# Performance work log

Measured on AMD Instinct MI355X. Metric: run time of the kernel, lower is better.

The kernel has to match this reference:

```python
import jax, jax.numpy as jnp
import numpy as np

B, S, V, F, H = 256, 512, 50000, 64, 256


def setup_inputs() -> dict:
    key = jax.random.key(0)
    ks = jax.random.split(key, 12)
    s_in = 1.0 / np.sqrt(F)
    s_hid = 1.0 / np.sqrt(H)
    return {
        "batch": jax.random.randint(ks[0], (B, S), 0, V),
        "features": jax.random.normal(ks[1], (V, F), jnp.float32),
        "W_ih0": jax.random.normal(ks[2], (H, F), jnp.float32) * s_in,
        "W_hh0": jax.random.normal(ks[3], (H, H), jnp.float32) * s_hid,
        "b_ih0": jax.random.normal(ks[4], (H,), jnp.float32) * s_hid,
        "b_hh0": jax.random.normal(ks[5], (H,), jnp.float32) * s_hid,
        "W_ih1": jax.random.normal(ks[6], (H, H), jnp.float32) * s_hid,
        "W_hh1": jax.random.normal(ks[7], (H, H), jnp.float32) * s_hid,
        "b_ih1": jax.random.normal(ks[8], (H,), jnp.float32) * s_hid,
        "b_hh1": jax.random.normal(ks[9], (H,), jnp.float32) * s_hid,
        "W_out": jax.random.normal(ks[10], (V, H), jnp.float32) * s_hid,
        "b_out": jax.random.normal(ks[11], (V,), jnp.float32) * s_hid,
    }


def _rnn_layer(x, W_ih, W_hh, b_ih, b_hh):
    # x: [B, S, Din] -> [B, S, H]; torch tanh RNN: h_t = tanh(x_t W_ih^T + b_ih + h_{t-1} W_hh^T + b_hh)
    xW = jnp.einsum('bsd,hd->bsh', x, W_ih) + (b_ih + b_hh)  # precompute input projection
    h0 = jnp.zeros((x.shape[0], W_hh.shape[0]), x.dtype)

    def step(h, xt):
        h = jnp.tanh(xt + h @ W_hh.T)
        return h, h

    _, ys = jax.lax.scan(step, h0, jnp.swapaxes(xW, 0, 1))  # scan over time
    return jnp.swapaxes(ys, 0, 1)


def reference(batch, features, W_ih0, W_hh0, b_ih0, b_hh0,
              W_ih1, W_hh1, b_ih1, b_hh1, W_out, b_out):
    # vectorized replacement of the nested per-token gather loop
    full_representation = features[batch]            # [B, S, F]
    h = _rnn_layer(full_representation, W_ih0, W_hh0, b_ih0, b_hh0)
    h = _rnn_layer(h, W_ih1, W_hh1, b_ih1, b_hh1)    # [B, S, H]
    return h[:, -1, :] @ W_out.T + b_out             # [B, V]
```

## Files before the change

kernel.cpp:

```cpp
#include <hip/hip_runtime.h>

#define B_ 256
#define S_ 512
#define V_ 50000
#define F_ 64
#define H_ 256

typedef _Float16 f16;
typedef _Float16 f16x2 __attribute__((ext_vector_type(2)));
typedef _Float16 f16x4 __attribute__((ext_vector_type(4)));
typedef _Float16 f16x8 __attribute__((ext_vector_type(8)));
typedef float f32x4 __attribute__((ext_vector_type(4)));

#define MFMA(a, b, c) __builtin_amdgcn_mfma_f32_16x16x32_f16((a), (b), (c), 0, 0, 0)

__device__ __forceinline__ f16x8 cvt8(const float4 a, const float4 b) {
    f16x8 v;
    v[0] = (f16)a.x; v[1] = (f16)a.y; v[2] = (f16)a.z; v[3] = (f16)a.w;
    v[4] = (f16)b.x; v[5] = (f16)b.y; v[6] = (f16)b.z; v[7] = (f16)b.w;
    return v;
}

__device__ __forceinline__ float fast_tanh(float x) {
    float e = __expf(2.f * x);
    float r = __builtin_amdgcn_rcpf(e + 1.f);
    return __builtin_fmaf(-2.f, r, 1.f);
}

__device__ __forceinline__ f32x4 cvt4f(const f16x4 v) {
    f32x4 r; r[0] = (float)v[0]; r[1] = (float)v[1]; r[2] = (float)v[2]; r[3] = (float)v[3];
    return r;
}
__device__ __forceinline__ f16x4 pack4(const f32x4 a, const f32x4 b) {
    f16x4 r; r[0] = (f16)(a[0] + b[0]); r[1] = (f16)(a[1] + b[1]);
    r[2] = (f16)(a[2] + b[2]); r[3] = (f16)(a[3] + b[3]);
    return r;
}
__device__ __forceinline__ f16x4 tanh4(const f32x4 a, const f32x4 b) {
    f16x4 r;
#pragma unroll
    for (int i = 0; i < 4; ++i) r[i] = (f16)fast_tanh(a[i] + b[i]);
    return r;
}

__global__ void k_init_flags(int* flags) {
    if (threadIdx.x < 256) flags[threadIdx.x] = 0;
}

__global__ __launch_bounds__(512) void k_vocab_proj(
    const float* __restrict__ feat, const float* __restrict__ Wih,
    const float* __restrict__ bi, const float* __restrict__ bh,
    f16* __restrict__ T)
{
    __shared__ char Wl[256 * 128];
    __shared__ char Xl[16 * 128];
    const int tid = threadIdx.x;
    {
        const int n = tid >> 1, k0 = (tid & 1) << 5;
#pragma unroll
        for (int k = k0; k < k0 + 32; k += 8) {
            float4 a = *(const float4*)(Wih + n * F_ + k);
            float4 b = *(const float4*)(Wih + n * F_ + k + 4);
            *(f16x8*)(Wl + n * 128 + (((k >> 3) ^ (n & 7)) << 4)) = cvt8(a, b);
        }
    }
    const int v0 = blockIdx.x * 16;
    {
        const int m = tid >> 5, k = (tid & 31) << 1;
        float2 a = *(const float2*)(feat + (v0 + m) * F_ + k);
        f16x2 v; v[0] = (f16)a.x; v[1] = (f16)a.y;
        *(f16x2*)(Xl + m * 128 + ((((k >> 3) ^ (m & 7)) << 4) | ((k & 7) << 1))) = v;
    }
    __syncthreads();
    const int lane = tid & 63, w = tid >> 6;
    const int q = lane & 15, g = lane >> 4;
#pragma unroll
    for (int nt = 0; nt < 2; ++nt) {
        const int n0 = w * 32 + nt * 16;
        const int nrow = n0 + q;
        float4 b1 = *(const float4*)(bi + n0 + g * 4);
        float4 b2 = *(const float4*)(bh + n0 + g * 4);
        f32x4 acc = {b1.x + b2.x, b1.y + b2.y, b1.z + b2.z, b1.w + b2.w};
#pragma unroll
        for (int kb = 0; kb < 2; ++kb) {
            f16x8 a = *(const f16x8*)(Wl + nrow * 128 + (((kb * 4 + g) ^ (nrow & 7)) << 4));
            f16x8 b = *(const f16x8*)(Xl + q * 128 + (((kb * 4 + g) ^ (q & 7)) << 4));
            acc = MFMA(a, b, acc);
        }
        f16x4 o; o[0] = (f16)acc[0]; o[1] = (f16)acc[1]; o[2] = (f16)acc[2]; o[3] = (f16)acc[3];
        *(f16x4*)(T + (size_t)(v0 + q) * H_ + n0 + g * 4) = o;
    }
}

__global__ __launch_bounds__(512) __attribute__((amdgpu_waves_per_eu(2, 2)))
void k_rnn2(
    const f16* __restrict__ T, const int* __restrict__ idx,
    const float* __restrict__ Whh0, const float* __restrict__ Wih1,
    const float* __restrict__ bih1, const float* __restrict__ bhh1,
    const float* __restrict__ Whh1,
    f16* __restrict__ h0ring, f16* __restrict__ plow,
    int* flags, f16* __restrict__ h1out)
{
    __shared__ char hb[2][8192];
    __shared__ char h0c[2][8192];
    __shared__ char pbb[2][4096];
    const int wg = blockIdx.x;
    const int tid = threadIdx.x, lane = tid & 63, w = tid >> 6;
    const int q = lane & 15, gl = lane >> 4;
    const int swz = (q & 7) << 4;

    int rbase[2];
#pragma unroll
    for (int p2 = 0; p2 < 2; ++p2)
        rbase[p2] = q * 512 + ((p2 * 64 + gl * 16) ^ swz);

    int* prodf = flags;
    int* consf = flags + 128;
    const int gr = (wg < 16) ? wg : wg - 16;
    const int brow = gr * 16 + q;
    f16* ringg = h0ring + ((size_t)gr << 19);

#define FRDB(base_, kb_) (*(const f16x8*)((base_) + rbase[(kb_) & 1] + (((kb_) >> 1) * 128)))
#define STEP_BAR() do { \
        asm volatile("s_waitcnt lgkmcnt(0)" ::: "memory"); \
        __builtin_amdgcn_s_barrier(); \
    } while (0)

    if (wg < 16) {
        const int nb2 = w * 32;
        const int pcol = w * 16;
        int wb2[2];
#pragma unroll
        for (int tt = 0; tt < 2; ++tt)
            wb2[tt] = q * 512 + (((nb2 + tt * 16 + gl * 4) * 2) ^ swz);

        f16x8 wA[2][8], wPl[8];
#pragma unroll
        for (int tt = 0; tt < 2; ++tt) {
            const int n = nb2 + tt * 16 + q;
#pragma unroll
            for (int kb = 0; kb < 8; ++kb) {
                const int o = n * H_ + kb * 32 + gl * 8;
                wA[tt][kb] = cvt8(*(const float4*)(Whh0 + o), *(const float4*)(Whh0 + o + 4));
            }
        }
#pragma unroll
        for (int kb = 0; kb < 8; ++kb) {
            const int o = (pcol + q) * H_ + kb * 32 + gl * 8;
            wPl[kb] = cvt8(*(const float4*)(Wih1 + o), *(const float4*)(Wih1 + o + 4));
        }
        f32x4 bsP;
        {
            const int n = pcol + gl * 4;
            float4 x = *(const float4*)(bih1 + n);
            float4 y = *(const float4*)(bhh1 + n);
            bsP[0] = x.x + y.x; bsP[1] = x.y + y.y; bsP[2] = x.z + y.z; bsP[3] = x.w + y.w;
        }
        {   f32x4 z = {0.f, 0.f, 0.f, 0.f}; *(f32x4*)(hb[1] + tid * 16) = z; }
        const int* idxr = idx + brow * S_;
        int* myflag = prodf + gr * 8 + w;
        f16x4 xa[2], xb[2];
        {
            const size_t r0 = (size_t)idxr[0] * H_, r1 = (size_t)idxr[1] * H_;
#pragma unroll
            for (int tt = 0; tt < 2; ++tt) {
                xa[tt] = *(const f16x4*)(T + r0 + nb2 + tt * 16 + gl * 4);
                xb[tt] = *(const f16x4*)(T + r1 + nb2 + tt * 16 + gl * 4);
            }
        }
        int iA = idxr[2], iB = idxr[3];
        __syncthreads();

#define PBODY(XV, ID, RD, WR, T_) do {                                          \
        if (((T_) & 15) == 0) {       \
            int v_;                                                             \
            do { v_ = __hip_atomic_load(consf + gr, __ATOMIC_RELAXED,           \
                                        __HIP_MEMORY_SCOPE_AGENT);              \
            } while ((T_) - v_ > 96);                                           \
        }                                                                       \
        f16x8 bf0 = FRDB(hb[RD], 0), bf1 = FRDB(hb[RD], 1), bf2 = FRDB(hb[RD], 2), \
              bf3 = FRDB(hb[RD], 3), bf4 = FRDB(hb[RD], 4), bf5 = FRDB(hb[RD], 5), \
              bf6 = FRDB(hb[RD], 6), bf7 = FRDB(hb[RD], 7);                     \
        f32x4 aL[2], aH[2];                                                     \
        _Pragma("unroll")                                                       \
        for (int tt = 0; tt < 2; ++tt) {                                        \
            aL[tt] = cvt4f(XV[tt]);                                             \
            aH[tt][0] = 0.f; aH[tt][1] = 0.f; aH[tt][2] = 0.f; aH[tt][3] = 0.f; \
        }                                                                       \
        if ((((T_) & 7) == 0) && lane == 0)                                     \
            __hip_atomic_store(myflag, (T_), __ATOMIC_RELEASE,                  \
                               __HIP_MEMORY_SCOPE_AGENT);                       \
        {                                                                       \
            const size_t rr = (size_t)ID * H_;                                  \
            _Pragma("unroll")                                                   \
            for (int tt = 0; tt < 2; ++tt)                                      \
                XV[tt] = *(const f16x4*)(T + rr + nb2 + tt * 16 + gl * 4);      \
            const int t4 = ((T_) + 4 < S_) ? (T_) + 4 : S_ - 1;                 \
            ID = idxr[t4];                                                      \
        }                                                                       \
        _Pragma("unroll")                                                       \
        for (int tt = 0; tt < 2; ++tt) {                                        \
            aL[tt] = MFMA(wA[tt][0], bf0, aL[tt]);                              \
            aH[tt] = MFMA(wA[tt][4], bf4, aH[tt]);                              \
            aL[tt] = MFMA(wA[tt][1], bf1, aL[tt]);                              \
            aH[tt] = MFMA(wA[tt][5], bf5, aH[tt]);                              \
            aL[tt] = MFMA(wA[tt][2], bf2, aL[tt]);                              \
            aH[tt] = MFMA(wA[tt][6], bf6, aH[tt]);                              \
            aL[tt] = MFMA(wA[tt][3], bf3, aL[tt]);                              \
            aH[tt] = MFMA(wA[tt][7], bf7, aH[tt]);                              \
        }                                                                       \
                    \
        f32x4 pLx = bsP, pHx;                                                   \
        pHx[0] = 0.f; pHx[1] = 0.f; pHx[2] = 0.f; pHx[3] = 0.f;                 \
        pLx = MFMA(wPl[0], bf0, pLx);  pHx = MFMA(wPl[4], bf4, pHx);            \
        pLx = MFMA(wPl[1], bf1, pLx);  pHx = MFMA(wPl[5], bf5, pHx);            \
        pLx = MFMA(wPl[2], bf2, pLx);  pHx = MFMA(wPl[6], bf6, pHx);            \
        pLx = MFMA(wPl[3], bf3, pLx);  pHx = MFMA(wPl[7], bf7, pHx);            \
        {                                                                       \
            f16* rp = ringg + (size_t)((T_) & 127) * 4096 + q * 256 + nb2;      \
            _Pragma("unroll")                                                   \
            for (int tt = 0; tt < 2; ++tt) {                                    \
                f16x4 hv = tanh4(aL[tt], aH[tt]);                               \
                *(f16x4*)(hb[WR] + wb2[tt]) = hv;                               \
                *(f16x4*)(rp + tt * 16 + gl * 4) = hv;                          \
            }                                                                   \
            *(f16x4*)(plow + ((size_t)brow * 512 + (T_) - 1) * 128              \
                      + pcol + gl * 4) = pack4(pLx, pHx);                       \
        }                                                                       \
        STEP_BAR();                                                             \
    } while (0)

        {
            f16x8 bf0 = FRDB(hb[1], 0), bf1 = FRDB(hb[1], 1), bf2 = FRDB(hb[1], 2),
                  bf3 = FRDB(hb[1], 3), bf4 = FRDB(hb[1], 4), bf5 = FRDB(hb[1], 5),
                  bf6 = FRDB(hb[1], 6), bf7 = FRDB(hb[1], 7);
            f32x4 aL[2], aH[2];
#pragma unroll
            for (int tt = 0; tt < 2; ++tt) {
                aL[tt] = cvt4f(xa[tt]);
                aH[tt][0] = 0.f; aH[tt][1] = 0.f; aH[tt][2] = 0.f; aH[tt][3] = 0.f;
            }
            {
                const size_t rr = (size_t)iA * H_;
#pragma unroll
                for (int tt = 0; tt < 2; ++tt)
                    xa[tt] = *(const f16x4*)(T + rr + nb2 + tt * 16 + gl * 4);
                iA = idxr[4];
            }
#pragma unroll
            for (int tt = 0; tt < 2; ++tt) {
                aL[tt] = MFMA(wA[tt][0], bf0, aL[tt]);
                aH[tt] = MFMA(wA[tt][4], bf4, aH[tt]);
                aL[tt] = MFMA(wA[tt][1], bf1, aL[tt]);
                aH[tt] = MFMA(wA[tt][5], bf5, aH[tt]);
                aL[tt] = MFMA(wA[tt][2], bf2, aL[tt]);
                aH[tt] = MFMA(wA[tt][6], bf6, aH[tt]);
                aL[tt] = MFMA(wA[tt][3], bf3, aL[tt]);
                aH[tt] = MFMA(wA[tt][7], bf7, aH[tt]);
            }
            f16* rp = ringg + q * 256 + nb2;
#pragma unroll
            for (int tt = 0; tt < 2; ++tt) {
                f16x4 hv = tanh4(aL[tt], aH[tt]);
                *(f16x4*)(hb[0] + wb2[tt]) = hv;
                *(f16x4*)(rp + tt * 16 + gl * 4) = hv;
            }
            STEP_BAR();
        }
        for (int t = 1; t < 511; t += 2) {
            PBODY(xb, iB, 0, 1, t);
            PBODY(xa, iA, 1, 0, t + 1);
        }
        PBODY(xb, iB, 0, 1, 511);
        {
            f16x8 bf0 = FRDB(hb[1], 0), bf1 = FRDB(hb[1], 1), bf2 = FRDB(hb[1], 2),
                  bf3 = FRDB(hb[1], 3), bf4 = FRDB(hb[1], 4), bf5 = FRDB(hb[1], 5),
                  bf6 = FRDB(hb[1], 6), bf7 = FRDB(hb[1], 7);
            f32x4 pLx = bsP, pHx;
            pHx[0] = 0.f; pHx[1] = 0.f; pHx[2] = 0.f; pHx[3] = 0.f;
            pLx = MFMA(wPl[0], bf0, pLx);  pHx = MFMA(wPl[4], bf4, pHx);
            pLx = MFMA(wPl[1], bf1, pLx);  pHx = MFMA(wPl[5], bf5, pHx);
            pLx = MFMA(wPl[2], bf2, pLx);  pHx = MFMA(wPl[6], bf6, pHx);
            pLx = MFMA(wPl[3], bf3, pLx);  pHx = MFMA(wPl[7], bf7, pHx);
            *(f16x4*)(plow + ((size_t)brow * 512 + 511) * 128 + pcol + gl * 4)
                = pack4(pLx, pHx);
        }
        if (lane == 0)
            __hip_atomic_store(myflag, 512, __ATOMIC_RELEASE, __HIP_MEMORY_SCOPE_AGENT);
#undef PBODY
    } else {
        const bool isC = (w < 4);
        const int stg_r = tid >> 5, stg_c = tid & 31;
        const int stg_addr = stg_r * 512 + ((stg_c ^ (stg_r & 7)) << 4);
        const int pj = w - 4;
        const int nb4 = w * 64;
        int xbase[4];
#pragma unroll
        for (int tt = 0; tt < 4; ++tt)
            xbase[tt] = q * 512 + ((((isC ? nb4 : 0) + tt * 16 + gl * 4) * 2) ^ swz);

        f16x8 wR[4][8];
        f32x4 bsPh[2];
        if (isC) {
#pragma unroll
            for (int tt = 0; tt < 4; ++tt) {
                const int n = nb4 + tt * 16 + q;
#pragma unroll
                for (int kb = 0; kb < 8; ++kb) {
                    const int o = n * H_ + kb * 32 + gl * 8;
                    wR[tt][kb] = cvt8(*(const float4*)(Whh1 + o), *(const float4*)(Whh1 + o + 4));
                }
            }
        } else {
#pragma unroll
            for (int tt = 0; tt < 2; ++tt) {
                const int n = 128 + pj * 32 + tt * 16 + q;
#pragma unroll
                for (int kb = 0; kb < 8; ++kb) {
                    const int o = n * H_ + kb * 32 + gl * 8;
                    wR[tt][kb] = cvt8(*(const float4*)(Wih1 + o), *(const float4*)(Wih1 + o + 4));
                }
                const int nb = 128 + pj * 32 + tt * 16 + gl * 4;
                float4 x = *(const float4*)(bih1 + nb);
                float4 y = *(const float4*)(bhh1 + nb);
                bsPh[tt][0] = x.x + y.x; bsPh[tt][1] = x.y + y.y;
                bsPh[tt][2] = x.z + y.z; bsPh[tt][3] = x.w + y.w;
            }
        }
        {   f32x4 z = {0.f, 0.f, 0.f, 0.f}; *(f32x4*)(hb[1] + tid * 16) = z; }

#define SPIN(need) do {                                                         \
        int mn_;                                                                \
        do {                                                                    \
            mn_ = 0x7fffffff;                                                   \
            _Pragma("unroll")                                                   \
            for (int i_ = 0; i_ < 8; ++i_) {                                    \
                int v_ = __hip_atomic_load(prodf + gr * 8 + i_, __ATOMIC_RELAXED, \
                                           __HIP_MEMORY_SCOPE_AGENT);           \
                mn_ = v_ < mn_ ? v_ : mn_;                                      \
            }                                                                   \
        } while (mn_ < (need));                                                 \
        __builtin_amdgcn_fence(__ATOMIC_ACQUIRE, "agent");                      \
    } while (0)

        f16x4 pvE[4], pvO[4];
        SPIN(13);
        {
            f16x8 sreg = *(const f16x8*)(ringg + (size_t)tid * 8);
            if (isC && w < 2) {
#pragma unroll
                for (int tt = 0; tt < 4; ++tt) {
                    pvE[tt] = *(const f16x4*)(plow + ((size_t)brow * 512 + 0) * 128
                                              + nb4 + tt * 16 + gl * 4);
                    pvO[tt] = *(const f16x4*)(plow + ((size_t)brow * 512 + 1) * 128
                                              + nb4 + tt * 16 + gl * 4);
                }
            }
            *(f16x8*)(h0c[0] + stg_addr) = sreg;
        }
        __syncthreads();

#define CSTEP(PV, PAR, S_) do {                                                 \
        if (((S_) & 7) == 1) {                                                  \
            const int nd_ = ((S_) + 11 < 512) ? (S_) + 11 : 512;                \
            SPIN(nd_);                                                          \
        }                                                                       \
        const int sl_ = ((S_) + 1 < 512) ? (S_) + 1 : 511;                      \
        f16x8 sreg = *(const f16x8*)(ringg + (size_t)(sl_ & 127) * 4096 + (size_t)tid * 8); \
        if (isC) {                                                              \
            f32x4 cL[4], cH[4];                                                 \
            if (w < 2) {                                                        \
                _Pragma("unroll")                                               \
                for (int tt = 0; tt < 4; ++tt) cL[tt] = cvt4f(PV[tt]);          \
            } else {                                                            \
                _Pragma("unroll")                                               \
                for (int tt = 0; tt < 4; ++tt) {                                \
                    f16x4 pv_ = *(const f16x4*)(pbb[1 - (PAR)]                  \
                        + ((16 * (w - 2) + 4 * tt + gl) * 16 + q) * 8);         \
                    cL[tt] = cvt4f(pv_);                                        \
                }                                                               \
            }                                                                   \
            _Pragma("unroll")                                                   \
            for (int tt = 0; tt < 4; ++tt) {                                    \
                cH[tt][0] = 0.f; cH[tt][1] = 0.f; cH[tt][2] = 0.f; cH[tt][3] = 0.f; \
            }                                                                   \
            f16x8 cf0 = FRDB(hb[PAR], 0), cf1 = FRDB(hb[PAR], 1),               \
                  cf2 = FRDB(hb[PAR], 2), cf3 = FRDB(hb[PAR], 3),               \
                  cf4 = FRDB(hb[PAR], 4), cf5 = FRDB(hb[PAR], 5),               \
                  cf6 = FRDB(hb[PAR], 6), cf7 = FRDB(hb[PAR], 7);               \
            _Pragma("unroll")                                                   \
            for (int tt = 0; tt < 4; ++tt) {                                    \
                cL[tt] = MFMA(wR[tt][0], cf0, cL[tt]);                          \
                cH[tt] = MFMA(wR[tt][4], cf4, cH[tt]);                          \
                cL[tt] = MFMA(wR[tt][1], cf1, cL[tt]);                          \
                cH[tt] = MFMA(wR[tt][5], cf5, cH[tt]);                          \
                cL[tt] = MFMA(wR[tt][2], cf2, cL[tt]);                          \
                cH[tt] = MFMA(wR[tt][6], cf6, cH[tt]);                          \
                cL[tt] = MFMA(wR[tt][3], cf3, cL[tt]);                          \
                cH[tt] = MFMA(wR[tt][7], cf7, cH[tt]);                          \
            }                                                                   \
            if (w < 2) {            \
                const int tr = ((S_) + 1 < 512) ? (S_) + 1 : 511;               \
                _Pragma("unroll")                                               \
                for (int tt = 0; tt < 4; ++tt)                                  \
                    PV[tt] = *(const f16x4*)(plow + ((size_t)brow * 512 + tr) * 128 \
                                             + nb4 + tt * 16 + gl * 4);         \
            }                                                                   \
            _Pragma("unroll")                                                   \
            for (int tt = 0; tt < 4; ++tt)                                      \
                *(f16x4*)(hb[1 - (PAR)] + xbase[tt]) = tanh4(cL[tt], cH[tt]);   \
            if ((tid == 0) && (((S_) & 15) == 0))                               \
                __hip_atomic_store(consf + gr, (S_), __ATOMIC_RELEASE,          \
                                   __HIP_MEMORY_SCOPE_AGENT);                   \
        } else {                                                                \
            f16x8 hf0 = FRDB(h0c[PAR], 0), hf1 = FRDB(h0c[PAR], 1),             \
                  hf2 = FRDB(h0c[PAR], 2), hf3 = FRDB(h0c[PAR], 3),             \
                  hf4 = FRDB(h0c[PAR], 4), hf5 = FRDB(h0c[PAR], 5),             \
                  hf6 = FRDB(h0c[PAR], 6), hf7 = FRDB(h0c[PAR], 7);             \
            f32x4 pL[2], pH[2];                                                 \
            _Pragma("unroll")                                                   \
            for (int tt = 0; tt < 2; ++tt) {                                    \
                pL[tt] = bsPh[tt];                                              \
                pH[tt][0] = 0.f; pH[tt][1] = 0.f; pH[tt][2] = 0.f; pH[tt][3] = 0.f; \
                pL[tt] = MFMA(wR[tt][0], hf0, pL[tt]);                          \
                pH[tt] = MFMA(wR[tt][4], hf4, pH[tt]);                          \
                pL[tt] = MFMA(wR[tt][1], hf1, pL[tt]);                          \
                pH[tt] = MFMA(wR[tt][5], hf5, pH[tt]);                          \
                pL[tt] = MFMA(wR[tt][2], hf2, pL[tt]);                          \
                pH[tt] = MFMA(wR[tt][6], hf6, pH[tt]);                          \
                pL[tt] = MFMA(wR[tt][3], hf3, pL[tt]);                          \
                pH[tt] = MFMA(wR[tt][7], hf7, pH[tt]);                          \
                *(f16x4*)(pbb[PAR] + ((8 * pj + 4 * tt + gl) * 16 + q) * 8)     \
                    = pack4(pL[tt], pH[tt]);                                    \
            }                                                                   \
        }                                                                       \
        *(f16x8*)(h0c[1 - (PAR)] + stg_addr) = sreg;                            \
        STEP_BAR();                                                             \
    } while (0)

        {
            f16x8 sreg = *(const f16x8*)(ringg + (size_t)4096 + (size_t)tid * 8);
            if (!isC) {
                f16x8 hf0 = FRDB(h0c[0], 0), hf1 = FRDB(h0c[0], 1),
                      hf2 = FRDB(h0c[0], 2), hf3 = FRDB(h0c[0], 3),
                      hf4 = FRDB(h0c[0], 4), hf5 = FRDB(h0c[0], 5),
                      hf6 = FRDB(h0c[0], 6), hf7 = FRDB(h0c[0], 7);
                f32x4 pL[2], pH[2];
#pragma unroll
                for (int tt = 0; tt < 2; ++tt) {
                    pL[tt] = bsPh[tt];
                    pH[tt][0] = 0.f; pH[tt][1] = 0.f; pH[tt][2] = 0.f; pH[tt][3] = 0.f;
                    pL[tt] = MFMA(wR[tt][0], hf0, pL[tt]);
                    pH[tt] = MFMA(wR[tt][4], hf4, pH[tt]);
                    pL[tt] = MFMA(wR[tt][1], hf1, pL[tt]);
                    pH[tt] = MFMA(wR[tt][5], hf5, pH[tt]);
                    pL[tt] = MFMA(wR[tt][2], hf2, pL[tt]);
                    pH[tt] = MFMA(wR[tt][6], hf6, pH[tt]);
                    pL[tt] = MFMA(wR[tt][3], hf3, pL[tt]);
                    pH[tt] = MFMA(wR[tt][7], hf7, pH[tt]);
                    *(f16x4*)(pbb[0] + ((8 * pj + 4 * tt + gl) * 16 + q) * 8)
                        = pack4(pL[tt], pH[tt]);
                }
            }
            *(f16x8*)(h0c[1] + stg_addr) = sreg;
            STEP_BAR();
        }
        for (int s = 1; s < 511; s += 2) {
            CSTEP(pvE, 1, s);
            CSTEP(pvO, 0, s + 1);
        }
        CSTEP(pvE, 1, 511);
        if (isC) {
            f32x4 cL[4], cH[4];
            if (w < 2) {
#pragma unroll
                for (int tt = 0; tt < 4; ++tt) cL[tt] = cvt4f(pvO[tt]);
            } else {
#pragma unroll
                for (int tt = 0; tt < 4; ++tt) {
                    f16x4 pv_ = *(const f16x4*)(pbb[1]
                        + ((16 * (w - 2) + 4 * tt + gl) * 16 + q) * 8);
                    cL[tt] = cvt4f(pv_);
                }
            }
#pragma unroll
            for (int tt = 0; tt < 4; ++tt) {
                cH[tt][0] = 0.f; cH[tt][1] = 0.f; cH[tt][2] = 0.f; cH[tt][3] = 0.f;
            }
            f16x8 cf0 = FRDB(hb[0], 0), cf1 = FRDB(hb[0], 1),
                  cf2 = FRDB(hb[0], 2), cf3 = FRDB(hb[0], 3),
                  cf4 = FRDB(hb[0], 4), cf5 = FRDB(hb[0], 5),
                  cf6 = FRDB(hb[0], 6), cf7 = FRDB(hb[0], 7);
#pragma unroll
            for (int tt = 0; tt < 4; ++tt) {
                cL[tt] = MFMA(wR[tt][0], cf0, cL[tt]);
                cH[tt] = MFMA(wR[tt][4], cf4, cH[tt]);
                cL[tt] = MFMA(wR[tt][1], cf1, cL[tt]);
                cH[tt] = MFMA(wR[tt][5], cf5, cH[tt]);
                cL[tt] = MFMA(wR[tt][2], cf2, cL[tt]);
                cH[tt] = MFMA(wR[tt][6], cf6, cH[tt]);
                cL[tt] = MFMA(wR[tt][3], cf3, cL[tt]);
                cH[tt] = MFMA(wR[tt][7], cf7, cH[tt]);
            }
#pragma unroll
            for (int tt = 0; tt < 4; ++tt)
                *(f16x4*)(h1out + (size_t)brow * H_ + nb4 + tt * 16 + gl * 4)
                    = tanh4(cL[tt], cH[tt]);
        }
        if (isC && tid == 0)
            __hip_atomic_store(consf + gr, 512, __ATOMIC_RELEASE, __HIP_MEMORY_SCOPE_AGENT);
#undef CSTEP
#undef SPIN
    }
#undef FRDB
#undef STEP_BAR
}

__global__ __launch_bounds__(512) void k_out(
    const f16* __restrict__ h1, const float* __restrict__ Wout,
    const float* __restrict__ bout, float* __restrict__ out)
{
    __shared__ char Hl[256 * 512];
    const int tid = threadIdx.x;
    {
        const int m = tid >> 1, half = tid & 1;
#pragma unroll
        for (int i = 0; i < 16; ++i) {
            const int blk = half * 16 + i;
            f16x8 v = *(const f16x8*)(h1 + m * H_ + blk * 8);
            *(f16x8*)(Hl + m * 512 + ((blk ^ (m & 7)) << 4)) = v;
        }
    }
    __syncthreads();
    const int lane = tid & 63, w = tid >> 6;
    const int q = lane & 15, g = lane >> 4;
    const int v0 = blockIdx.x * 80;
    f32x4 acc[5][2];
#pragma unroll
    for (int vt = 0; vt < 5; ++vt) {
        float4 bo = *(const float4*)(bout + v0 + vt * 16 + g * 4);
#pragma unroll
        for (int bt = 0; bt < 2; ++bt) {
            acc[vt][bt][0] = bo.x; acc[vt][bt][1] = bo.y;
            acc[vt][bt][2] = bo.z; acc[vt][bt][3] = bo.w;
        }
    }
#pragma unroll
    for (int kb = 0; kb < 8; ++kb) {
        f16x8 bf[2];
#pragma unroll
        for (int bt = 0; bt < 2; ++bt) {
            const int mrow = (w * 2 + bt) * 16 + q;
            bf[bt] = *(const f16x8*)(Hl + mrow * 512 + (((kb * 4 + g) ^ (mrow & 7)) << 4));
        }
#pragma unroll
        for (int vt = 0; vt < 5; ++vt) {
            const size_t vrow = v0 + vt * 16 + q;
            float4 a = *(const float4*)(Wout + vrow * H_ + kb * 32 + g * 8);
            float4 b = *(const float4*)(Wout + vrow * H_ + kb * 32 + g * 8 + 4);
            f16x8 af = cvt8(a, b);
#pragma unroll
            for (int bt = 0; bt < 2; ++bt)
                acc[vt][bt] = MFMA(af, bf[bt], acc[vt][bt]);
        }
    }
#pragma unroll
    for (int vt = 0; vt < 5; ++vt)
#pragma unroll
        for (int bt = 0; bt < 2; ++bt) {
            const int b = (w * 2 + bt) * 16 + q;
            const int v = v0 + vt * 16 + g * 4;
            float4 o = {acc[vt][bt][0], acc[vt][bt][1], acc[vt][bt][2], acc[vt][bt][3]};
            *(float4*)(out + (size_t)b * V_ + v) = o;
        }
}

extern "C" void kernel_launch(void* const* d_in, const int* in_sizes, int n_in,
                              void* d_out, int out_size, void* d_ws, size_t ws_size,
                              hipStream_t stream) {
    (void)in_sizes; (void)n_in; (void)out_size; (void)ws_size;
    const int*   batch = (const int*)  d_in[0];
    const float* feat  = (const float*)d_in[1];
    const float* Wih0  = (const float*)d_in[2];
    const float* Whh0  = (const float*)d_in[3];
    const float* bih0  = (const float*)d_in[4];
    const float* bhh0  = (const float*)d_in[5];
    const float* Wih1  = (const float*)d_in[6];
    const float* Whh1  = (const float*)d_in[7];
    const float* bih1  = (const float*)d_in[8];
    const float* bhh1  = (const float*)d_in[9];
    const float* Wout  = (const float*)d_in[10];
    const float* bout  = (const float*)d_in[11];
    float* out = (float*)d_out;

    f16* T      = (f16*)d_out;
    f16* h0ring = (f16*)((char*)d_out + 27000000);
    int* flags  = (int*)((char*)d_out + 48000000);
    f16* plow   = (f16*)d_ws;
    f16* h1out  = (f16*)((char*)d_ws + (size_t)B_ * S_ * 128 * 2);

    k_init_flags<<<dim3(1), dim3(256), 0, stream>>>(flags);
    k_vocab_proj<<<dim3(V_ / 16), dim3(512), 0, stream>>>(feat, Wih0, bih0, bhh0, T);
    k_rnn2<<<dim3(32), dim3(512), 0, stream>>>(T, batch, Whh0, Wih1, bih1, bhh1,
                                               Whh1, h0ring, plow, flags, h1out);
    k_out<<<dim3(625), dim3(512), 0, stream>>>(h1out, Wout, bout, out);
}
```

Measured before the change: 1.028 ms.

## Load layer-0 hidden state from ring directly into registers, drop LDS staging

In the layer-1 consumer workgroups, the projection waves now read the h0 ring buffer straight from global memory into register fragments (HF) one step ahead. This replaces the earlier path of staging through a shared h0c buffer with a cooperative store and per-step LDS reads. The pbb buffer now uses the same swizzled xbase layout for both its writers and readers. In the producer step, the plow projection MFMAs are moved after the tanh/ring stores so the hidden state is published earlier. The change cuts LDS traffic and per-step staging work, but adds global-load latency to every step and more register pressure.

```diff
diff --git a/kernel.cpp b/kernel.cpp
--- a/kernel.cpp
+++ b/kernel.cpp
@@ -102,8 +102,7 @@
     int* flags, f16* __restrict__ h1out)
 {
     __shared__ char hb[2][8192];
-    __shared__ char h0c[2][8192];
-    __shared__ char pbb[2][4096];
+    __shared__ char pbb[2][8192];
     const int wg = blockIdx.x;
     const int tid = threadIdx.x, lane = tid & 63, w = tid >> 6;
     const int q = lane & 15, gl = lane >> 4;
@@ -209,14 +208,7 @@
             aL[tt] = MFMA(wA[tt][3], bf3, aL[tt]);                              \
             aH[tt] = MFMA(wA[tt][7], bf7, aH[tt]);                              \
         }                                                                       \
-                    \
-        f32x4 pLx = bsP, pHx;                                                   \
-        pHx[0] = 0.f; pHx[1] = 0.f; pHx[2] = 0.f; pHx[3] = 0.f;                 \
-        pLx = MFMA(wPl[0], bf0, pLx);  pHx = MFMA(wPl[4], bf4, pHx);            \
-        pLx = MFMA(wPl[1], bf1, pLx);  pHx = MFMA(wPl[5], bf5, pHx);            \
-        pLx = MFMA(wPl[2], bf2, pLx);  pHx = MFMA(wPl[6], bf6, pHx);            \
-        pLx = MFMA(wPl[3], bf3, pLx);  pHx = MFMA(wPl[7], bf7, pHx);            \
-        {                                                                       \
+        {             \
             f16* rp = ringg + (size_t)((T_) & 127) * 4096 + q * 256 + nb2;      \
             _Pragma("unroll")                                                   \
             for (int tt = 0; tt < 2; ++tt) {                                    \
@@ -224,6 +216,14 @@
                 *(f16x4*)(hb[WR] + wb2[tt]) = hv;                               \
                 *(f16x4*)(rp + tt * 16 + gl * 4) = hv;                          \
             }                                                                   \
+        }                                                                       \
+        {                                                                       \
+            f32x4 pLx = bsP, pHx;                                               \
+            pHx[0] = 0.f; pHx[1] = 0.f; pHx[2] = 0.f; pHx[3] = 0.f;             \
+            pLx = MFMA(wPl[0], bf0, pLx);  pHx = MFMA(wPl[4], bf4, pHx);        \
+            pLx = MFMA(wPl[1], bf1, pLx);  pHx = MFMA(wPl[5], bf5, pHx);        \
+            pLx = MFMA(wPl[2], bf2, pLx);  pHx = MFMA(wPl[6], bf6, pHx);        \
+            pLx = MFMA(wPl[3], bf3, pLx);  pHx = MFMA(wPl[7], bf7, pHx);        \
             *(f16x4*)(plow + ((size_t)brow * 512 + (T_) - 1) * 128              \
                       + pcol + gl * 4) = pack4(pLx, pHx);                       \
         }                                                                       \
@@ -290,14 +290,13 @@
 #undef PBODY
     } else {
         const bool isC = (w < 4);
-        const int stg_r = tid >> 5, stg_c = tid & 31;
-        const int stg_addr = stg_r * 512 + ((stg_c ^ (stg_r & 7)) << 4);
         const int pj = w - 4;
         const int nb4 = w * 64;
+        const int nbP = 128 + pj * 32;
         int xbase[4];
 #pragma unroll
         for (int tt = 0; tt < 4; ++tt)
-            xbase[tt] = q * 512 + ((((isC ? nb4 : 0) + tt * 16 + gl * 4) * 2) ^ swz);
+            xbase[tt] = q * 512 + ((((isC ? nb4 : nbP) + tt * 16 + gl * 4) * 2) ^ swz);
 
         f16x8 wR[4][8];
         f32x4 bsPh[2];
@@ -314,13 +313,13 @@
         } else {
 #pragma unroll
             for (int tt = 0; tt < 2; ++tt) {
-                const int n = 128 + pj * 32 + tt * 16 + q;
+                const int n = nbP + tt * 16 + q;
 #pragma unroll
                 for (int kb = 0; kb < 8; ++kb) {
                     const int o = n * H_ + kb * 32 + gl * 8;
                     wR[tt][kb] = cvt8(*(const float4*)(Wih1 + o), *(const float4*)(Wih1 + o + 4));
                 }
-                const int nb = 128 + pj * 32 + tt * 16 + gl * 4;
+                const int nb = nbP + tt * 16 + gl * 4;
                 float4 x = *(const float4*)(bih1 + nb);
                 float4 y = *(const float4*)(bhh1 + nb);
                 bsPh[tt][0] = x.x + y.x; bsPh[tt][1] = x.y + y.y;
@@ -344,19 +343,22 @@
     } while (0)
 
         f16x4 pvE[4], pvO[4];
+        f16x8 HF[8];
         SPIN(13);
-        {
-            f16x8 sreg = *(const f16x8*)(ringg + (size_t)tid * 8);
-            if (isC && w < 2) {
-#pragma unroll
-                for (int tt = 0; tt < 4; ++tt) {
-                    pvE[tt] = *(const f16x4*)(plow + ((size_t)brow * 512 + 0) * 128
-                                              + nb4 + tt * 16 + gl * 4);
-                    pvO[tt] = *(const f16x4*)(plow + ((size_t)brow * 512 + 1) * 128
-                                              + nb4 + tt * 16 + gl * 4);
-                }
-            }
-            *(f16x8*)(h0c[0] + stg_addr) = sreg;
+        if (isC && w < 2) {
+#pragma unroll
+            for (int tt = 0; tt < 4; ++tt) {
+                pvE[tt] = *(const f16x4*)(plow + ((size_t)brow * 512 + 0) * 128
+                                          + nb4 + tt * 16 + gl * 4);
+                pvO[tt] = *(const f16x4*)(plow + ((size_t)brow * 512 + 1) * 128
+                                          + nb4 + tt * 16 + gl * 4);
+            }
+        }
+        if (!isC) {
+            const f16* rp = ringg + q * 256 + gl * 8;
+#pragma unroll
+            for (int kb = 0; kb < 8; ++kb)
+                HF[kb] = *(const f16x8*)(rp + kb * 32);
         }
         __syncthreads();
 
@@ -365,8 +367,6 @@
             const int nd_ = ((S_) + 11 < 512) ? (S_) + 11 : 512;                \
             SPIN(nd_);                                                          \
         }                                                                       \
-        const int sl_ = ((S_) + 1 < 512) ? (S_) + 1 : 511;                      \
-        f16x8 sreg = *(const f16x8*)(ringg + (size_t)(sl_ & 127) * 4096 + (size_t)tid * 8); \
         if (isC) {                                                              \
             f32x4 cL[4], cH[4];                                                 \
             if (w < 2) {                                                        \
@@ -375,8 +375,7 @@
             } else {                                                            \
                 _Pragma("unroll")                                               \
                 for (int tt = 0; tt < 4; ++tt) {                                \
-                    f16x4 pv_ = *(const f16x4*)(pbb[1 - (PAR)]                  \
-                        + ((16 * (w - 2) + 4 * tt + gl) * 16 + q) * 8);         \
+                    f16x4 pv_ = *(const f16x4*)(pbb[1 - (PAR)] + xbase[tt]);    \
                     cL[tt] = cvt4f(pv_);                                        \
                 }                                                               \
             }                                                                   \
@@ -413,56 +412,60 @@
                 __hip_atomic_store(consf + gr, (S_), __ATOMIC_RELEASE,          \
                                    __HIP_MEMORY_SCOPE_AGENT);                   \
         } else {                                                                \
-            f16x8 hf0 = FRDB(h0c[PAR], 0), hf1 = FRDB(h0c[PAR], 1),             \
-                  hf2 = FRDB(h0c[PAR], 2), hf3 = FRDB(h0c[PAR], 3),             \
-                  hf4 = FRDB(h0c[PAR], 4), hf5 = FRDB(h0c[PAR], 5),             \
-                  hf6 = FRDB(h0c[PAR], 6), hf7 = FRDB(h0c[PAR], 7);             \
             f32x4 pL[2], pH[2];                                                 \
             _Pragma("unroll")                                                   \
             for (int tt = 0; tt < 2; ++tt) {                                    \
                 pL[tt] = bsPh[tt];                                              \
                 pH[tt][0] = 0.f; pH[tt][1] = 0.f; pH[tt][2] = 0.f; pH[tt][3] = 0.f; \
-                pL[tt] = MFMA(wR[tt][0], hf0, pL[tt]);                          \
-                pH[tt] = MFMA(wR[tt][4], hf4, pH[tt]);                          \
-                pL[tt] = MFMA(wR[tt][1], hf1, pL[tt]);                          \
-                pH[tt] = MFMA(wR[tt][5], hf5, pH[tt]);                          \
-                pL[tt] = MFMA(wR[tt][2], hf2, pL[tt]);                          \
-                pH[tt] = MFMA(wR[tt][6], hf6, pH[tt]);                          \
-                pL[tt] = MFMA(wR[tt][3], hf3, pL[tt]);                          \
-                pH[tt] = MFMA(wR[tt][7], hf7, pH[tt]);                          \
-                *(f16x4*)(pbb[PAR] + ((8 * pj + 4 * tt + gl) * 16 + q) * 8)     \
-                    = pack4(pL[tt], pH[tt]);                                    \
-            }                                                                   \
-        }                                                                       \
-        *(f16x8*)(h0c[1 - (PAR)] + stg_addr) = sreg;                            \
+                pL[tt] = MFMA(wR[tt][0], HF[0], pL[tt]);                        \
+                pH[tt] = MFMA(wR[tt][4], HF[4], pH[tt]);                        \
+                pL[tt] = MFMA(wR[tt][1], HF[1], pL[tt]);                        \
+                pH[tt] = MFMA(wR[tt][5], HF[5], pH[tt]);                        \
+                pL[tt] = MFMA(wR[tt][2], HF[2], pL[tt]);                        \
+                pH[tt] = MFMA(wR[tt][6], HF[6], pH[tt]);                        \
+                pL[tt] = MFMA(wR[tt][3], HF[3], pL[tt]);                        \
+                pH[tt] = MFMA(wR[tt][7], HF[7], pH[tt]);                        \
+            }                                                                   \
+            {              \
+                const int nx = ((S_) + 1 < 512) ? (S_) + 1 : 511;               \
+                const f16* rp = ringg + (size_t)(nx & 127) * 4096 + q * 256 + gl * 8; \
+                _Pragma("unroll")                                               \
+                for (int kb = 0; kb < 8; ++kb)                                  \
+                    HF[kb] = *(const f16x8*)(rp + kb * 32);                     \
+            }                                                                   \
+            _Pragma("unroll")                                                   \
+            for (int tt = 0; tt < 2; ++tt)                                      \
+                *(f16x4*)(pbb[PAR] + xbase[tt]) = pack4(pL[tt], pH[tt]);        \
+        }                                                                       \
         STEP_BAR();                                                             \
     } while (0)
 
         {
-            f16x8 sreg = *(const f16x8*)(ringg + (size_t)4096 + (size_t)tid * 8);
             if (!isC) {
-                f16x8 hf0 = FRDB(h0c[0], 0), hf1 = FRDB(h0c[0], 1),
-                      hf2 = FRDB(h0c[0], 2), hf3 = FRDB(h0c[0], 3),
-                      hf4 = FRDB(h0c[0], 4), hf5 = FRDB(h0c[0], 5),
-                      hf6 = FRDB(h0c[0], 6), hf7 = FRDB(h0c[0], 7);
                 f32x4 pL[2], pH[2];
 #pragma unroll
                 for (int tt = 0; tt < 2; ++tt) {
                     pL[tt] = bsPh[tt];
                     pH[tt][0] = 0.f; pH[tt][1] = 0.f; pH[tt][2] = 0.f; pH[tt][3] = 0.f;
-                    pL[tt] = MFMA(wR[tt][0], hf0, pL[tt]);
-                    pH[tt] = MFMA(wR[tt][4], hf4, pH[tt]);
-                    pL[tt] = MFMA(wR[tt][1], hf1, pL[tt]);
-                    pH[tt] = MFMA(wR[tt][5], hf5, pH[tt]);
-                    pL[tt] = MFMA(wR[tt][2], hf2, pL[tt]);
-                    pH[tt] = MFMA(wR[tt][6], hf6, pH[tt]);
-                    pL[tt] = MFMA(wR[tt][3], hf3, pL[tt]);
-                    pH[tt] = MFMA(wR[tt][7], hf7, pH[tt]);
-                    *(f16x4*)(pbb[0] + ((8 * pj + 4 * tt + gl) * 16 + q) * 8)
-                        = pack4(pL[tt], pH[tt]);
+                    pL[tt] = MFMA(wR[tt][0], HF[0], pL[tt]);
+                    pH[tt] = MFMA(wR[tt][4], HF[4], pH[tt]);
+                    pL[tt] = MFMA(wR[tt][1], HF[1], pL[tt]);
+                    pH[tt] = MFMA(wR[tt][5], HF[5], pH[tt]);
+                    pL[tt] = MFMA(wR[tt][2], HF[2], pL[tt]);
+                    pH[tt] = MFMA(wR[tt][6], HF[6], pH[tt]);
+                    pL[tt] = MFMA(wR[tt][3], HF[3], pL[tt]);
+                    pH[tt] = MFMA(wR[tt][7], HF[7], pH[tt]);
                 }
-            }
-            *(f16x8*)(h0c[1] + stg_addr) = sreg;
+                {
+                    const f16* rp = ringg + (size_t)4096 + q * 256 + gl * 8;
+#pragma unroll
+                    for (int kb = 0; kb < 8; ++kb)
+                        HF[kb] = *(const f16x8*)(rp + kb * 32);
+                }
+#pragma unroll
+                for (int tt = 0; tt < 2; ++tt)
+                    *(f16x4*)(pbb[0] + xbase[tt]) = pack4(pL[tt], pH[tt]);
+            }
             STEP_BAR();
         }
         for (int s = 1; s < 511; s += 2) {
@@ -478,8 +481,7 @@
             } else {
 #pragma unroll
                 for (int tt = 0; tt < 4; ++tt) {
-                    f16x4 pv_ = *(const f16x4*)(pbb[1]
-                        + ((16 * (w - 2) + 4 * tt + gl) * 16 + q) * 8);
+                    f16x4 pv_ = *(const f16x4*)(pbb[1] + xbase[tt]);
                     cL[tt] = cvt4f(pv_);
                 }
             }
```

Result: slower. 1.452 ms (+41.3%).
